# Performance work log

Measured on AMD Instinct MI355X. Metric: run time of the kernel, lower is better.

## Reference

```python
import jax, jax.numpy as jnp
import numpy as np

N = 100000      # user + item nodes
E = 600000      # number of edges
LATDIM = 128
HEAD = 4
HDIM = LATDIM // HEAD


def setup_inputs() -> dict:
    key = jax.random.key(0)
    ks = jax.random.split(key, 7)
    return {
        "embeds": jax.random.normal(ks[0], (N, LATDIM), dtype=jnp.float32),
        "qTrans": jax.random.normal(ks[1], (LATDIM, LATDIM), dtype=jnp.float32) * (1.0 / np.sqrt(LATDIM)),
        "kTrans": jax.random.normal(ks[2], (LATDIM, LATDIM), dtype=jnp.float32) * (1.0 / np.sqrt(LATDIM)),
        "vTrans": jax.random.normal(ks[3], (LATDIM, LATDIM), dtype=jnp.float32) * (1.0 / np.sqrt(LATDIM)),
        "filt": jax.random.normal(ks[4], (N, HEAD), dtype=jnp.float32),
        "rows": jax.random.randint(ks[5], (E,), 0, N, dtype=jnp.int32),
        "cols": jax.random.randint(ks[6], (E,), 0, N, dtype=jnp.int32),
    }


def reference(embeds, qTrans, kTrans, vTrans, filt, rows, cols):
    # gather endpoint embeddings: [E, latdim]
    rowEmbeds = embeds[rows]
    colEmbeds = embeds[cols]
    # per-edge multi-head q/k/v: [E, H, D]
    qEmbeds = (rowEmbeds @ qTrans).reshape(E, HEAD, HDIM)
    kEmbeds = (colEmbeds @ kTrans).reshape(E, HEAD, HDIM)
    vEmbeds = (colEmbeds @ vTrans).reshape(E, HEAD, HDIM)
    # per-edge per-head attention logits
    att = jnp.einsum('ehd,ehd->eh', qEmbeds, kEmbeds)
    att = jnp.clip(att, -10.0, 10.0)
    att = att + filt[cols]
    expAtt = jnp.exp(att)
    # segment softmax over destination rows
    attNorm = jax.ops.segment_sum(expAtt, rows, num_segments=N)[rows]
    att = expAtt / (attNorm + 1e-8)
    # weighted values, scatter-sum back to nodes
    resEdges = (att[:, :, None] * vEmbeds).reshape(E, LATDIM)
    resEmbeds = jax.ops.segment_sum(resEdges, rows, num_segments=N)
    return resEmbeds
```

## Files before the change

kernel.cpp:

```cpp
#include <hip/hip_runtime.h>

#define N_NODES 100000
#define E_EDGES 600000
#define LATDIM 128
#define HEAD 4
#define HDIM 32

#define SCAN_NB 98

typedef _Float16 f16x8 __attribute__((ext_vector_type(8)));
typedef float    f32x4 __attribute__((ext_vector_type(4)));

__device__ __forceinline__ unsigned f32_to_bf16_rne(float x) {
    unsigned u = __float_as_uint(x);
    u += 0x7fffu + ((u >> 16) & 1u);
    return u >> 16;
}

__global__ __launch_bounds__(256) void wprep_kernel(
    const float* __restrict__ qT, const float* __restrict__ kT,
    const float* __restrict__ vT,
    unsigned short* __restrict__ WT,
    int* __restrict__ counts, unsigned* __restrict__ state)
{
    int g = blockIdx.x * 256 + threadIdx.x;

    for (int i = g; i < N_NODES; i += SCAN_NB * 256) counts[i] = 0;
    if (g < 128) state[g] = 0u;

    if (g >= 3072) return;
    int m    = g >> 10;
    int rem  = g & 1023;
    int c    = rem >> 3;
    int k0   = (rem & 7) * 16;
    const float* W = (m == 0) ? qT : (m == 1) ? kT : vT;

    unsigned short hv[16];
    #pragma unroll
    for (int j = 0; j < 16; ++j) {
        _Float16 h = (_Float16)W[(size_t)(k0 + j) * 128 + c];
        hv[j] = __builtin_bit_cast(unsigned short, h);
    }
    size_t off = (size_t)m * 16384 + (size_t)c * 128 + k0;
    *(uint4*)(WT + off)     = *(const uint4*)&hv[0];
    *(uint4*)(WT + off + 8) = *(const uint4*)&hv[8];
}

__global__ __launch_bounds__(256) void qkv_mfma_kernel(
    const float* __restrict__ embeds,
    const unsigned short* __restrict__ WT,
    const int* __restrict__ rows,
    int* __restrict__ counts,
    float* __restrict__ Q, unsigned* __restrict__ KV)
{
    __shared__ __align__(16) char smem[32768];
    char* R0 = smem;
    char* R1 = smem + 16384;

    const int tid = threadIdx.x;
    const int rowBase = blockIdx.x * 64;

    uint4 pb0, pb1, pb2, pb3;

#define PF(MN, HN) do {                                                          \
        const char* _s = (const char*)(WT + (size_t)(MN) * 16384                 \
                                          + (size_t)(HN) * 8192);                \
        pb0 = *(const uint4*)(_s + (size_t)(0 * 256 + tid) * 16);                \
        pb1 = *(const uint4*)(_s + (size_t)(1 * 256 + tid) * 16);                \
        pb2 = *(const uint4*)(_s + (size_t)(2 * 256 + tid) * 16);                \
        pb3 = *(const uint4*)(_s + (size_t)(3 * 256 + tid) * 16);                \
    } while (0)

#define COMMIT(R) do {                                                           \
        { int _i = 0 * 256 + tid; int _c = _i >> 4;                              \
          int _s = (_c * 256 + (_i & 15) * 16) ^ ((_c & 7) << 4);                \
          *(uint4*)((R) + _s) = pb0; }                                           \
        { int _i = 1 * 256 + tid; int _c = _i >> 4;                              \
          int _s = (_c * 256 + (_i & 15) * 16) ^ ((_c & 7) << 4);                \
          *(uint4*)((R) + _s) = pb1; }                                           \
        { int _i = 2 * 256 + tid; int _c = _i >> 4;                              \
          int _s = (_c * 256 + (_i & 15) * 16) ^ ((_c & 7) << 4);                \
          *(uint4*)((R) + _s) = pb2; }                                           \
        { int _i = 3 * 256 + tid; int _c = _i >> 4;                              \
          int _s = (_c * 256 + (_i & 15) * 16) ^ ((_c & 7) << 4);                \
          *(uint4*)((R) + _s) = pb3; }                                           \
    } while (0)

#define MFMA_M(ACC, R) do {                                                      \
        _Pragma("unroll")                                                        \
        for (int kk = 0; kk < 4; ++kk) {                                         \
            _Pragma("unroll")                                                    \
            for (int n = 0; n < 4; ++n) {                                        \
                int col  = n * 16 + lrow;                                        \
                int byte = (col * 256 + kk * 64 + kg * 16) ^ ((lrow & 7) << 4);  \
                f16x8 b = __builtin_bit_cast(f16x8, *(const uint4*)((R) + byte)); \
                ACC[n] = __builtin_amdgcn_mfma_f32_16x16x32_f16(a[kk], b, ACC[n], 0, 0, 0); \
            }                                                                    \
        }                                                                        \
    } while (0)

#define ZACC(ACC) f32x4 ACC[4] = { {0.f,0.f,0.f,0.f}, {0.f,0.f,0.f,0.f},         \
                                   {0.f,0.f,0.f,0.f}, {0.f,0.f,0.f,0.f} }

#define STORE_Q(ACC, H) do {                                                     \
        _Pragma("unroll")                                                        \
        for (int n = 0; n < 4; ++n)                                              \
        _Pragma("unroll")                                                        \
        for (int j = 0; j < 4; ++j) {                                            \
            int gr  = rowBase + wv * 16 + kg * 4 + j;                            \
            int col = (H) * 64 + n * 16 + lrow;                                  \
            if (gr < N_NODES) Q[(size_t)gr * 128 + col] = ACC[n][j];             \
        }                                                                        \
    } while (0)

#define STORE_KV(ACC, H) do {                                                    \
        _Pragma("unroll")                                                        \
        for (int n = 0; n < 4; ++n)                                              \
        _Pragma("unroll")                                                        \
        for (int j = 0; j < 4; ++j) {                                            \
            int gr  = rowBase + wv * 16 + kg * 4 + j;                            \
            int col = (H) * 64 + n * 16 + lrow;                                  \
            if (gr < N_NODES) {                                                  \
                unsigned pk = f32_to_bf16_rne(kreg[n][j])                        \
                            | (f32_to_bf16_rne(ACC[n][j]) << 16);                \
                KV[(size_t)gr * 128 + col] = pk;                                 \
            }                                                                    \
        }                                                                        \
    } while (0)

    PF(0, 0);

    #pragma unroll
    for (int it = 0; it < 4; ++it) {
        int idx = it * 256 + tid;
        int r   = idx >> 4;
        int c16 = idx & 15;
        int gr  = rowBase + r;
        float4 u0 = make_float4(0.f, 0.f, 0.f, 0.f), u1 = u0;
        if (gr < N_NODES) {
            const float* p = embeds + (size_t)gr * 128 + c16 * 8;
            u0 = *(const float4*)p;
            u1 = *(const float4*)(p + 4);
        }
        f16x8 v;
        v[0] = (_Float16)u0.x; v[1] = (_Float16)u0.y;
        v[2] = (_Float16)u0.z; v[3] = (_Float16)u0.w;
        v[4] = (_Float16)u1.x; v[5] = (_Float16)u1.y;
        v[6] = (_Float16)u1.z; v[7] = (_Float16)u1.w;
        int byte = (r * 256 + c16 * 16) ^ ((r & 7) << 4);
        *(uint4*)(R0 + byte) = __builtin_bit_cast(uint4, v);
    }
    __syncthreads();

    const int lane = tid & 63;
    const int wv   = tid >> 6;
    const int lrow = lane & 15;
    const int kg   = lane >> 4;

    f16x8 a[4];
    {
        const int arow = wv * 16 + lrow;
        #pragma unroll
        for (int kk = 0; kk < 4; ++kk) {
            int byte = (arow * 256 + kk * 64 + kg * 16) ^ ((lrow & 7) << 4);
            a[kk] = __builtin_bit_cast(f16x8, *(const uint4*)(R0 + byte));
        }
    }
    COMMIT(R1);
    __syncthreads();

    f32x4 kreg[4];

    {
        PF(1, 0); ZACC(acc);
        MFMA_M(acc, R1);
        STORE_Q(acc, 0);
        COMMIT(R0); __syncthreads();
    }
    {
        PF(2, 0); ZACC(acc);
        MFMA_M(acc, R0);
        kreg[0] = acc[0]; kreg[1] = acc[1]; kreg[2] = acc[2]; kreg[3] = acc[3];
        COMMIT(R1); __syncthreads();
    }
    {
        PF(0, 1); ZACC(acc);
        MFMA_M(acc, R1);
        STORE_KV(acc, 0);
        COMMIT(R0); __syncthreads();
    }
    {
        PF(1, 1); ZACC(acc);
        MFMA_M(acc, R0);
        STORE_Q(acc, 1);
        COMMIT(R1); __syncthreads();
    }
    {
        PF(2, 1); ZACC(acc);
        MFMA_M(acc, R1);
        kreg[0] = acc[0]; kreg[1] = acc[1]; kreg[2] = acc[2]; kreg[3] = acc[3];
        COMMIT(R0); __syncthreads();
    }
    {
        ZACC(acc);
        MFMA_M(acc, R0);
        STORE_KV(acc, 1);
    }

    for (int e = blockIdx.x * 256 + tid; e < E_EDGES; e += gridDim.x * 256)
        atomicAdd(&counts[rows[e]], 1);

#undef PF
#undef COMMIT
#undef MFMA_M
#undef ZACC
#undef STORE_Q
#undef STORE_KV
}

__global__ __launch_bounds__(256) void scan_lb_kernel(
    const int* __restrict__ counts, int* __restrict__ starts,
    int* __restrict__ cursor, unsigned* __restrict__ state)
{
    __shared__ int s[256];
    __shared__ int bcast;
    int b = blockIdx.x, t = threadIdx.x;
    int base = b * 1024 + t * 4;
    int v0 = (base + 0 < N_NODES) ? counts[base + 0] : 0;
    int v1 = (base + 1 < N_NODES) ? counts[base + 1] : 0;
    int v2 = (base + 2 < N_NODES) ? counts[base + 2] : 0;
    int v3 = (base + 3 < N_NODES) ? counts[base + 3] : 0;
    int local = v0 + v1 + v2 + v3;
    s[t] = local;
    __syncthreads();
    for (int off = 1; off < 256; off <<= 1) {
        int x = (t >= off) ? s[t - off] : 0;
        __syncthreads();
        s[t] += x;
        __syncthreads();
    }
    int incl  = s[t];
    int excl  = incl - local;
    int total = s[255];

    if (t == 0) {
        int sum = 0;
        if (b == 0) {
            atomicExch(&state[0], ((unsigned)total << 2) | 2u);
        } else {
            atomicExch(&state[b], ((unsigned)total << 2) | 1u);
            int i = b - 1;
            while (true) {
                unsigned w = atomicAdd(&state[i], 0u);
                unsigned st = w & 3u;
                if (st == 0u) continue;
                sum += (int)(w >> 2);
                if (st == 2u) break;
                --i;
            }
            atomicExch(&state[b], ((unsigned)(sum + total) << 2) | 2u);
        }
        bcast = sum;
    }
    __syncthreads();
    int e = excl + bcast;
    if (base + 0 < N_NODES) { starts[base + 0] = e;                cursor[base + 0] = e; }
    if (base + 1 < N_NODES) { starts[base + 1] = e + v0;           cursor[base + 1] = e + v0; }
    if (base + 2 < N_NODES) { starts[base + 2] = e + v0 + v1;      cursor[base + 2] = e + v0 + v1; }
    if (base + 3 < N_NODES) { starts[base + 3] = e + v0 + v1 + v2; cursor[base + 3] = e + v0 + v1 + v2; }
}

__global__ __launch_bounds__(256) void scatter_kernel(
    const int* __restrict__ rows, const int* __restrict__ cols,
    int* __restrict__ cursor, int* __restrict__ csrCols)
{
    int e = blockIdx.x * 256 + threadIdx.x;
    if (e >= E_EDGES) return;
    int pos = atomicAdd(&cursor[rows[e]], 1);
    csrCols[pos] = cols[e];
}

__global__ __launch_bounds__(256) void att_agg_kernel(
    const float* __restrict__ Q, const unsigned* __restrict__ KV,
    const float* __restrict__ filt,
    const int* __restrict__ starts, const int* __restrict__ counts,
    const int* __restrict__ csrCols,
    float* __restrict__ out)
{
    int t = threadIdx.x;
    int node = blockIdx.x * 8 + (t >> 5);
    if (node >= N_NODES) return;
    int lane = t & 31;
    int h = lane >> 3;

    float4 q = ((const float4*)(Q + (size_t)node * 128))[lane];
    int s   = starts[node];
    int cnt = counts[node];

    float norm = 0.f;
    float ax = 0.f, ay = 0.f, az = 0.f, aw = 0.f;

#define EDGE_BODY(KVU, F)                                                     \
    {                                                                          \
        float kx = __uint_as_float((KVU).x << 16), vx = __uint_as_float((KVU).x & 0xffff0000u); \
        float ky = __uint_as_float((KVU).y << 16), vy = __uint_as_float((KVU).y & 0xffff0000u); \
        float kz = __uint_as_float((KVU).z << 16), vz = __uint_as_float((KVU).z & 0xffff0000u); \
        float kw = __uint_as_float((KVU).w << 16), vw = __uint_as_float((KVU).w & 0xffff0000u); \
        float p = q.x * kx + q.y * ky + q.z * kz + q.w * kw;                   \
        p += __shfl_xor(p, 1);                                                 \
        p += __shfl_xor(p, 2);                                                 \
        p += __shfl_xor(p, 4);                                                 \
        float w = __expf(fminf(fmaxf(p, -10.f), 10.f) + (F));                  \
        norm += w;                                                             \
        ax += w * vx; ay += w * vy; az += w * vz; aw += w * vw;                \
    }

    int i = 0;
    for (; i + 4 <= cnt; i += 4) {
        int c0 = csrCols[s + i];
        int c1 = csrCols[s + i + 1];
        int c2 = csrCols[s + i + 2];
        int c3 = csrCols[s + i + 3];
        uint4 kv0 = ((const uint4*)KV)[(size_t)c0 * 32 + lane];
        uint4 kv1 = ((const uint4*)KV)[(size_t)c1 * 32 + lane];
        uint4 kv2 = ((const uint4*)KV)[(size_t)c2 * 32 + lane];
        uint4 kv3 = ((const uint4*)KV)[(size_t)c3 * 32 + lane];
        float f0 = filt[c0 * HEAD + h];
        float f1 = filt[c1 * HEAD + h];
        float f2 = filt[c2 * HEAD + h];
        float f3 = filt[c3 * HEAD + h];
        EDGE_BODY(kv0, f0);
        EDGE_BODY(kv1, f1);
        EDGE_BODY(kv2, f2);
        EDGE_BODY(kv3, f3);
    }
    for (; i < cnt; ++i) {
        int c0 = csrCols[s + i];
        uint4 kv0 = ((const uint4*)KV)[(size_t)c0 * 32 + lane];
        float f0 = filt[c0 * HEAD + h];
        EDGE_BODY(kv0, f0);
    }
#undef EDGE_BODY

    float inv = 1.0f / (norm + 1e-8f);
    ((float4*)(out + (size_t)node * 128))[lane] =
        make_float4(ax * inv, ay * inv, az * inv, aw * inv);
}

extern "C" void kernel_launch(void* const* d_in, const int* in_sizes, int n_in,
                              void* d_out, int out_size, void* d_ws, size_t ws_size,
                              hipStream_t stream) {
    const float* embeds = (const float*)d_in[0];
    const float* qT     = (const float*)d_in[1];
    const float* kT     = (const float*)d_in[2];
    const float* vT     = (const float*)d_in[3];
    const float* filt   = (const float*)d_in[4];
    const int*   rows   = (const int*)d_in[5];
    const int*   cols   = (const int*)d_in[6];
    float*       out    = (float*)d_out;

    float*    Q  = (float*)d_ws;
    unsigned* KV = (unsigned*)(Q + (size_t)N_NODES * 128);
    int* counts    = (int*)(KV + (size_t)N_NODES * 128);
    int* starts    = counts + N_NODES;
    int* cursor    = starts + N_NODES;
    int* csrCols   = cursor + N_NODES;
    unsigned* state = (unsigned*)(csrCols + E_EDGES);

    unsigned short* WT = (unsigned short*)csrCols;

    wprep_kernel<<<SCAN_NB, 256, 0, stream>>>(qT, kT, vT, WT, counts, state);
    qkv_mfma_kernel<<<(N_NODES + 63) / 64, 256, 0, stream>>>(
        embeds, WT, rows, counts, Q, KV);
    scan_lb_kernel<<<SCAN_NB, 256, 0, stream>>>(counts, starts, cursor, state);
    scatter_kernel<<<(E_EDGES + 255) / 256, 256, 0, stream>>>(rows, cols, cursor, csrCols);
    att_agg_kernel<<<(N_NODES + 7) / 8, 256, 0, stream>>>(
        Q, KV, filt, starts, counts, csrCols, out);
}
```

Before: 251.1 us.

## Store Q and K in fp16, use fdot2, and double-buffer edge gathers

Q is now stored as fp16 instead of fp32, which halves its write and read traffic. K is stored as fp16 and V as bf16 in a regrouped per-lane layout, so each lane gets 4 K and 4 V values in one 16-byte load. The logit dot product uses packed fp16 dot2 instructions. The aggregation loop is restructured into a two-buffer software pipeline that issues the next group's gathers before consuming the current group, with clamped indices and masking replacing the scalar tail loop. The cost is reduced precision for Q and K, plus some redundant loads for nodes whose degree is not a multiple of four.

```diff
diff --git a/kernel.cpp b/kernel.cpp
--- a/kernel.cpp
+++ b/kernel.cpp
@@ -9,12 +9,35 @@
 #define SCAN_NB 98
 
 typedef _Float16 f16x8 __attribute__((ext_vector_type(8)));
+typedef _Float16 f16x2 __attribute__((ext_vector_type(2)));
 typedef float    f32x4 __attribute__((ext_vector_type(4)));
 
 __device__ __forceinline__ unsigned f32_to_bf16_rne(float x) {
     unsigned u = __float_as_uint(x);
     u += 0x7fffu + ((u >> 16) & 1u);
     return u >> 16;
+}
+
+__device__ __forceinline__ float dot4_f16(unsigned k01, unsigned k23,
+                                          unsigned q01, unsigned q23) {
+#if defined(__has_builtin)
+#if __has_builtin(__builtin_amdgcn_fdot2)
+    float r = __builtin_amdgcn_fdot2(__builtin_bit_cast(f16x2, k01),
+                                     __builtin_bit_cast(f16x2, q01), 0.f, false);
+    return  __builtin_amdgcn_fdot2(__builtin_bit_cast(f16x2, k23),
+                                   __builtin_bit_cast(f16x2, q23), r, false);
+#else
+    f16x2 a = __builtin_bit_cast(f16x2, k01), b = __builtin_bit_cast(f16x2, q01);
+    f16x2 c = __builtin_bit_cast(f16x2, k23), d = __builtin_bit_cast(f16x2, q23);
+    return (float)a[0]*(float)b[0] + (float)a[1]*(float)b[1]
+         + (float)c[0]*(float)d[0] + (float)c[1]*(float)d[1];
+#endif
+#else
+    f16x2 a = __builtin_bit_cast(f16x2, k01), b = __builtin_bit_cast(f16x2, q01);
+    f16x2 c = __builtin_bit_cast(f16x2, k23), d = __builtin_bit_cast(f16x2, q23);
+    return (float)a[0]*(float)b[0] + (float)a[1]*(float)b[1]
+         + (float)c[0]*(float)d[0] + (float)c[1]*(float)d[1];
+#endif
 }
 
 __global__ __launch_bounds__(256) void wprep_kernel(
@@ -51,7 +74,7 @@
     const unsigned short* __restrict__ WT,
     const int* __restrict__ rows,
     int* __restrict__ counts,
-    float* __restrict__ Q, unsigned* __restrict__ KV)
+    unsigned short* __restrict__ Qh, char* __restrict__ KVb)
 {
     __shared__ __align__(16) char smem[32768];
     char* R0 = smem;
@@ -109,7 +132,9 @@
         for (int j = 0; j < 4; ++j) {                                            \
             int gr  = rowBase + wv * 16 + kg * 4 + j;                            \
             int col = (H) * 64 + n * 16 + lrow;                                  \
-            if (gr < N_NODES) Q[(size_t)gr * 128 + col] = ACC[n][j];             \
+            if (gr < N_NODES)                                                    \
+                Qh[(size_t)gr * 128 + col] =                                     \
+                    __builtin_bit_cast(unsigned short, (_Float16)ACC[n][j]);     \
         }                                                                        \
     } while (0)
 
@@ -121,9 +146,11 @@
             int gr  = rowBase + wv * 16 + kg * 4 + j;                            \
             int col = (H) * 64 + n * 16 + lrow;                                  \
             if (gr < N_NODES) {                                                  \
-                unsigned pk = f32_to_bf16_rne(kreg[n][j])                        \
-                            | (f32_to_bf16_rne(ACC[n][j]) << 16);                \
-                KV[(size_t)gr * 128 + col] = pk;                                 \
+                char* _b = KVb + (size_t)gr * 512 + (col >> 2) * 16 + (col & 3) * 2; \
+                *(unsigned short*)_b =                                           \
+                    __builtin_bit_cast(unsigned short, (_Float16)kreg[n][j]);    \
+                *(unsigned short*)(_b + 8) =                                     \
+                    (unsigned short)f32_to_bf16_rne(ACC[n][j]);                  \
             }                                                                    \
         }                                                                        \
     } while (0)
@@ -281,7 +308,7 @@
 }
 
 __global__ __launch_bounds__(256) void att_agg_kernel(
-    const float* __restrict__ Q, const unsigned* __restrict__ KV,
+    const unsigned short* __restrict__ Qh, const char* __restrict__ KVb,
     const float* __restrict__ filt,
     const int* __restrict__ starts, const int* __restrict__ counts,
     const int* __restrict__ csrCols,
@@ -293,54 +320,73 @@
     int lane = t & 31;
     int h = lane >> 3;
 
-    float4 q = ((const float4*)(Q + (size_t)node * 128))[lane];
-    int s   = starts[node];
-    int cnt = counts[node];
+    uint2 qp = *(const uint2*)(Qh + (size_t)node * 128 + lane * 4);
+    int s    = starts[node];
+    int cnt  = counts[node];
+    int last = cnt - 1;
 
     float norm = 0.f;
     float ax = 0.f, ay = 0.f, az = 0.f, aw = 0.f;
 
-#define EDGE_BODY(KVU, F)                                                     \
-    {                                                                          \
-        float kx = __uint_as_float((KVU).x << 16), vx = __uint_as_float((KVU).x & 0xffff0000u); \
-        float ky = __uint_as_float((KVU).y << 16), vy = __uint_as_float((KVU).y & 0xffff0000u); \
-        float kz = __uint_as_float((KVU).z << 16), vz = __uint_as_float((KVU).z & 0xffff0000u); \
-        float kw = __uint_as_float((KVU).w << 16), vw = __uint_as_float((KVU).w & 0xffff0000u); \
-        float p = q.x * kx + q.y * ky + q.z * kz + q.w * kw;                   \
-        p += __shfl_xor(p, 1);                                                 \
-        p += __shfl_xor(p, 2);                                                 \
-        p += __shfl_xor(p, 4);                                                 \
-        float w = __expf(fminf(fmaxf(p, -10.f), 10.f) + (F));                  \
-        norm += w;                                                             \
-        ax += w * vx; ay += w * vy; az += w * vz; aw += w * vw;                \
-    }
-
-    int i = 0;
-    for (; i + 4 <= cnt; i += 4) {
-        int c0 = csrCols[s + i];
-        int c1 = csrCols[s + i + 1];
-        int c2 = csrCols[s + i + 2];
-        int c3 = csrCols[s + i + 3];
-        uint4 kv0 = ((const uint4*)KV)[(size_t)c0 * 32 + lane];
-        uint4 kv1 = ((const uint4*)KV)[(size_t)c1 * 32 + lane];
-        uint4 kv2 = ((const uint4*)KV)[(size_t)c2 * 32 + lane];
-        uint4 kv3 = ((const uint4*)KV)[(size_t)c3 * 32 + lane];
-        float f0 = filt[c0 * HEAD + h];
-        float f1 = filt[c1 * HEAD + h];
-        float f2 = filt[c2 * HEAD + h];
-        float f3 = filt[c3 * HEAD + h];
-        EDGE_BODY(kv0, f0);
-        EDGE_BODY(kv1, f1);
-        EDGE_BODY(kv2, f2);
-        EDGE_BODY(kv3, f3);
-    }
-    for (; i < cnt; ++i) {
-        int c0 = csrCols[s + i];
-        uint4 kv0 = ((const uint4*)KV)[(size_t)c0 * 32 + lane];
-        float f0 = filt[c0 * HEAD + h];
-        EDGE_BODY(kv0, f0);
-    }
-#undef EDGE_BODY
+    int   a_c0, a_c1, a_c2, a_c3,  b_c0, b_c1, b_c2, b_c3;
+    float a_f0, a_f1, a_f2, a_f3,  b_f0, b_f1, b_f2, b_f3;
+    uint4 a_k0, a_k1, a_k2, a_k3,  b_k0, b_k1, b_k2, b_k3;
+
+#define LOADB(P, I) do {                                                        \
+        int _i1 = (I) + 1 < last ? (I) + 1 : last;                              \
+        int _i2 = (I) + 2 < last ? (I) + 2 : last;                              \
+        int _i3 = (I) + 3 < last ? (I) + 3 : last;                              \
+        P##_c0 = csrCols[s + (I)];  P##_c1 = csrCols[s + _i1];                  \
+        P##_c2 = csrCols[s + _i2];  P##_c3 = csrCols[s + _i3];                  \
+        P##_k0 = *(const uint4*)(KVb + (size_t)P##_c0 * 512 + lane * 16);       \
+        P##_k1 = *(const uint4*)(KVb + (size_t)P##_c1 * 512 + lane * 16);       \
+        P##_k2 = *(const uint4*)(KVb + (size_t)P##_c2 * 512 + lane * 16);       \
+        P##_k3 = *(const uint4*)(KVb + (size_t)P##_c3 * 512 + lane * 16);       \
+        P##_f0 = filt[P##_c0 * HEAD + h];  P##_f1 = filt[P##_c1 * HEAD + h];    \
+        P##_f2 = filt[P##_c2 * HEAD + h];  P##_f3 = filt[P##_c3 * HEAD + h];    \
+    } while (0)
+
+#define EDGE(KVU, F, VALID) {                                                   \
+        float p = dot4_f16((KVU).x, (KVU).y, qp.x, qp.y);                       \
+        float v0f = __uint_as_float((KVU).z << 16);                             \
+        float v1f = __uint_as_float((KVU).z & 0xffff0000u);                     \
+        float v2f = __uint_as_float((KVU).w << 16);                             \
+        float v3f = __uint_as_float((KVU).w & 0xffff0000u);                     \
+        p += __shfl_xor(p, 1);                                                  \
+        p += __shfl_xor(p, 2);                                                  \
+        p += __shfl_xor(p, 4);                                                  \
+        float w = __expf(fminf(fmaxf(p, -10.f), 10.f) + (F));                   \
+        w = (VALID) ? w : 0.f;                                                  \
+        norm += w;                                                              \
+        ax += w * v0f; ay += w * v1f; az += w * v2f; aw += w * v3f; }
+
+#define CONSUME(P, I) do {                                                      \
+        bool _m1 = (I) + 1 <= last;                                             \
+        bool _m2 = (I) + 2 <= last;                                             \
+        bool _m3 = (I) + 3 <= last;                                             \
+        EDGE(P##_k0, P##_f0, true);                                             \
+        EDGE(P##_k1, P##_f1, _m1);                                              \
+        EDGE(P##_k2, P##_f2, _m2);                                              \
+        EDGE(P##_k3, P##_f3, _m3);                                              \
+    } while (0)
+
+    if (cnt > 0) {
+        LOADB(a, 0);
+        int i = 0;
+        while (true) {
+            if (i + 4 < cnt) LOADB(b, i + 4);
+            CONSUME(a, i);
+            i += 4;
+            if (i >= cnt) break;
+            if (i + 4 < cnt) LOADB(a, i + 4);
+            CONSUME(b, i);
+            i += 4;
+            if (i >= cnt) break;
+        }
+    }
+#undef LOADB
+#undef EDGE
+#undef CONSUME
 
     float inv = 1.0f / (norm + 1e-8f);
     ((float4*)(out + (size_t)node * 128))[lane] =
@@ -359,9 +405,9 @@
     const int*   cols   = (const int*)d_in[6];
     float*       out    = (float*)d_out;
 
-    float*    Q  = (float*)d_ws;
-    unsigned* KV = (unsigned*)(Q + (size_t)N_NODES * 128);
-    int* counts    = (int*)(KV + (size_t)N_NODES * 128);
+    unsigned short* Qh = (unsigned short*)d_ws;
+    char* KVb      = (char*)(Qh + (size_t)N_NODES * 128);
+    int* counts    = (int*)(KVb + (size_t)N_NODES * 512);
     int* starts    = counts + N_NODES;
     int* cursor    = starts + N_NODES;
     int* csrCols   = cursor + N_NODES;
@@ -371,9 +417,9 @@
 
     wprep_kernel<<<SCAN_NB, 256, 0, stream>>>(qT, kT, vT, WT, counts, state);
     qkv_mfma_kernel<<<(N_NODES + 63) / 64, 256, 0, stream>>>(
-        embeds, WT, rows, counts, Q, KV);
+        embeds, WT, rows, counts, Qh, KVb);
     scan_lb_kernel<<<SCAN_NB, 256, 0, stream>>>(counts, starts, cursor, state);
     scatter_kernel<<<(E_EDGES + 255) / 256, 256, 0, stream>>>(rows, cols, cursor, csrCols);
     att_agg_kernel<<<(N_NODES + 7) / 8, 256, 0, stream>>>(
-        Q, KV, filt, starts, counts, csrCols, out);
-}
+        Qh, KVb, filt, starts, counts, csrCols, out);
+}
```

After: 250.0 us. No clear change (-0.5%).
